# Kernel optimization log

Measured on AMD Instinct MI355X. Metric: run time of the kernel, lower is better.

The kernel has to match this reference:

```python
import jax, jax.numpy as jnp
import numpy as np

# decoded layout constants
NN, NO, SD = 16, 8, 4          # num_neighbors, num_obstacles, state_dim_per_agent
B = 131072                      # batch rows
H1, E, HP, AD = 64, 16, 64, 2   # phi hidden, embed, psi hidden, action dim
D_ROBOT, D_OBST = 0.3, 0.3
B_GAMMA, B_EXPH = 0.05, 1.0
PHI_MIN, PHI_MAX = -2.0, 2.0
A_MAX = 2.0


def setup_inputs() -> dict:
    key = jax.random.key(0)
    kx, kw = jax.random.split(key)
    # x: [count | goal(SD) | NN neighbor rel-states (SD each) | NO obstacle rel-pos (2 each)]
    x = jax.random.normal(kx, (B, 1 + SD + SD * NN + 2 * NO), dtype=jnp.float32) * 2.0
    x = x.at[:, 0].set(float(NN))
    names = [("Wp1n", (SD, H1)), ("bp1n", (H1,)), ("Wp2n", (H1, E)), ("bp2n", (E,)),
             ("Wr1n", (E, H1)), ("br1n", (H1,)), ("Wr2n", (H1, E)), ("br2n", (E,)),
             ("Wp1o", (2, H1)), ("bp1o", (H1,)), ("Wp2o", (H1, E)), ("bp2o", (E,)),
             ("Wr1o", (E, H1)), ("br1o", (H1,)), ("Wr2o", (H1, E)), ("br2o", (E,)),
             ("Wpsi1", (2 * E + SD, HP)), ("bpsi1", (HP,)), ("Wpsi2", (HP, AD)), ("bpsi2", (AD,))]
    ks = jax.random.split(kw, len(names))
    inp = {"x": x}
    for (n, sh), k in zip(names, ks):
        s = 1.0 / np.sqrt(sh[0])  # torch Linear default init scale
        inp[n] = jax.random.uniform(k, sh, jnp.float32, -s, s)
    return inp


def _mlp2(h, W1, b1, W2, b2):
    # Feedforward: activation between layers, linear output
    return jax.nn.relu(h @ W1 + b1) @ W2 + b2


def _deepset(el, Wp1, bp1, Wp2, bp2, Wr1, br1, Wr2, br2):
    # el: [B, n, d] -> phi each element, sum over set, rho
    phi = _mlp2(el, Wp1, bp1, Wp2, bp2)          # [B, n, E]
    return _mlp2(phi.sum(axis=1), Wr1, br1, Wr2, br2)  # [B, E]


def _barrier_sum(P, D):
    # P: [B, n, 2]; APF barrier gamma * P / (|P| * (|P|-D)^exph), summed over n
    nrm = jnp.linalg.norm(P, axis=-1, keepdims=True)   # [B, n, 1]
    H = nrm - D
    return (B_GAMMA * P / (nrm * H ** B_EXPH)).sum(axis=1)  # [B, 2]


def reference(x, Wp1n, bp1n, Wp2n, bp2n, Wr1n, br1n, Wr2n, br2n,
              Wp1o, bp1o, Wp2o, bp2o, Wr1o, br1o, Wr2o, br2o,
              Wpsi1, bpsi1, Wpsi2, bpsi2):
    nb = x.shape[0]
    g = x[:, 1:1 + SD]                                        # goal
    nbr = x[:, 1 + SD:1 + SD + SD * NN].reshape(nb, NN, SD)   # neighbor rel-states
    obs = x[:, 1 + SD + SD * NN:].reshape(nb, NO, 2)          # obstacle rel-pos

    rho_n = _deepset(nbr, Wp1n, bp1n, Wp2n, bp2n, Wr1n, br1n, Wr2n, br2n)
    rho_o = _deepset(obs, Wp1o, bp1o, Wp2o, bp2o, Wr1o, br1o, Wr2o, br2o)

    h = jnp.concatenate([rho_n, rho_o, g], axis=1)            # [B, 2E+SD]
    emp = _mlp2(h, Wpsi1, bpsi1, Wpsi2, bpsi2)                # psi network
    emp = (jnp.tanh(emp) + 1.0) / 2.0 * (PHI_MAX - PHI_MIN) + PHI_MIN  # scale_empty

    bar = _barrier_sum(-nbr[:, :, :2], D_ROBOT) + _barrier_sum(-obs, D_OBST)

    action = emp + bar
    # scale(): divide rows whose inf-norm exceeds a_max
    inv_alpha = jnp.maximum(jnp.max(jnp.abs(action), axis=1, keepdims=True) / A_MAX, 1.0)
    return action / inv_alpha
```

## Files before the change

### kernel.cpp

```cpp
#include <hip/hip_runtime.h>
#include <math.h>


typedef __attribute__((ext_vector_type(8))) _Float16 f16x8;
typedef __attribute__((ext_vector_type(2))) __fp16 fp16x2;
typedef __attribute__((ext_vector_type(4))) float f32x4;

#define XW 85
#define WPB 4

#define FR_S1N  0
#define FR_S1O  4
#define FR_G2N  8
#define FR_G2O  10
#define FR_RNA  12
#define FR_RNB  16
#define FR_ROA  18
#define FR_ROB  22
#define FR_PSI1 24
#define FR_PSI2 32
#define N_FRAGS 34

#define BIG_STR 144
#define PHI_STR 80
#define CAT_STR 144
#define L_BIG 0
#define L_PHI 2304
#define L_CAT 3584
#define L_OUT 5888
#define L_BAR 6016
#define WAVE_LDS 6144

__device__ __forceinline__ float fast_rcp(float x)  { return __builtin_amdgcn_rcpf(x); }
__device__ __forceinline__ float fast_sqrt(float x) { return __builtin_amdgcn_sqrtf(x); }

__device__ __forceinline__ float two_tanh(float a) {
    float ax = fabsf(a);
    float e = __expf(2.0f * ax);
    float t = 1.0f - 2.0f * fast_rcp(e + 1.0f);
    return copysignf(2.0f * t, a);
}

__device__ __forceinline__ void lds_order() {
    __asm__ __volatile__("" ::: "memory");
}

__device__ __forceinline__ unsigned pk2(float a, float b) {
    union { fp16x2 h; unsigned u; } t;
    t.h = __builtin_amdgcn_cvt_pkrtz(a, b);
    return t.u;
}
__device__ __forceinline__ f16x8 make_a4(float f0, float f1, float f2, float f3) {
    union { unsigned u[4]; f16x8 v; } U;
    U.u[0] = pk2(f0, f1); U.u[1] = pk2(f2, f3); U.u[2] = 0; U.u[3] = 0;
    return U.v;
}
__device__ __forceinline__ f16x8 make_a2(float f0, float f1) {
    union { unsigned u[4]; f16x8 v; } U;
    U.u[0] = pk2(f0, f1); U.u[1] = 0; U.u[2] = 0; U.u[3] = 0;
    return U.v;
}
__device__ __forceinline__ f16x8 lds_af(const char* area, int stride, int off, int lane) {
    int mm = lane & 15, qq = lane >> 4;
    return *(const f16x8*)(area + mm * stride + off + qq * 16);
}
__device__ __forceinline__ f16x8 load_bh(const _Float16* wsf, int frag, int lane) {
    return ((const f16x8*)(wsf + (size_t)frag * 512))[lane];
}
__device__ __forceinline__ f32x4 cinit(float b) {
    f32x4 c; c[0] = b; c[1] = b; c[2] = b; c[3] = b; return c;
}
__device__ __forceinline__ f32x4 mfma1(f16x8 a, f16x8 b, f32x4 c) {
    return __builtin_amdgcn_mfma_f32_16x16x32_f16(a, b, c, 0, 0, 0);
}

__global__ void bn_prep(const float* __restrict__ Wp1n, const float* __restrict__ Wp2n,
                        const float* __restrict__ Wr1n, const float* __restrict__ Wr2n,
                        const float* __restrict__ Wp1o, const float* __restrict__ Wp2o,
                        const float* __restrict__ Wr1o, const float* __restrict__ Wr2o,
                        const float* __restrict__ Wpsi1, const float* __restrict__ Wpsi2,
                        _Float16* __restrict__ wsf)
{
    int f = blockIdx.x;
    int lane = threadIdx.x;
    const float* W; int K, N, kk = 0, nt = 0, rel;
    if (f < 4)        { W = Wp1n;  K = 4;  N = 64; nt = f; }
    else if (f < 8)   { W = Wp1o;  K = 2;  N = 64; nt = f - 4; }
    else if (f < 10)  { W = Wp2n;  K = 64; N = 16; kk = f - 8; }
    else if (f < 12)  { W = Wp2o;  K = 64; N = 16; kk = f - 10; }
    else if (f < 16)  { W = Wr1n;  K = 16; N = 64; nt = f - 12; }
    else if (f < 18)  { W = Wr2n;  K = 64; N = 16; kk = f - 16; }
    else if (f < 22)  { W = Wr1o;  K = 16; N = 64; nt = f - 18; }
    else if (f < 24)  { W = Wr2o;  K = 64; N = 16; kk = f - 22; }
    else if (f < 32)  { rel = f - 24; W = Wpsi1; K = 36; N = 64; kk = rel >> 2; nt = rel & 3; }
    else              { W = Wpsi2; K = 64; N = 2;  kk = f - 32; }

    int q = lane >> 4, c = lane & 15;
    _Float16* dst = wsf + (size_t)f * 512 + lane * 8;
    for (int j = 0; j < 8; ++j) {
        int k = kk * 32 + q * 8 + j;
        int n = nt * 16 + c;
        float v = (k < K && n < N) ? W[k * N + n] : 0.f;
        dst[j] = (_Float16)v;
    }
}

__global__ __launch_bounds__(256) void bn_main(
    const float* __restrict__ x, const _Float16* __restrict__ wsf,
    const float* __restrict__ bp1n, const float* __restrict__ bp2n,
    const float* __restrict__ br1n, const float* __restrict__ br2n,
    const float* __restrict__ bp1o, const float* __restrict__ bp2o,
    const float* __restrict__ br1o, const float* __restrict__ br2o,
    const float* __restrict__ bpsi1, const float* __restrict__ bpsi2,
    float* __restrict__ out, int nb)
{
    __shared__ char smem[WPB * WAVE_LDS];
    const int lane = threadIdx.x & 63;
    const int wid  = threadIdx.x >> 6;
    const int group = blockIdx.x * WPB + wid;
    const int row0 = group * 16;
    if (row0 >= nb) return;

    char* Wl   = smem + wid * WAVE_LDS;
    char* BIG  = Wl + L_BIG;
    char* PHI  = Wl + L_PHI;
    char* CAT  = Wl + L_CAT;
    char* OUTA = Wl + L_OUT;
    char* BAR  = Wl + L_BAR;

    const int m = lane & 15, q = lane >> 4, c = m;
    const float* xrow = x + (size_t)(row0 + m) * XW;

    for (int i = lane; i < 128; i += 64) {
        int r = i >> 3, d = i & 7;
        *(unsigned*)(PHI + r * PHI_STR + 32 + d * 4) = 0;
    }
    for (int i = lane; i < 256; i += 64) {
        int r = i >> 4, d = i & 15;
        *(unsigned*)(CAT + r * CAT_STR + 64 + d * 4) = 0;
    }
    lds_order();

    {
        float bx = 0.f, by = 0.f;
        #pragma unroll
        for (int i = 0; i < 4; ++i) {
            int n = 4 * q + i;
            float px = -xrow[5 + 4 * n], py = -xrow[6 + 4 * n];
            float nrm = fast_sqrt(px * px + py * py);
            float coef = 0.05f * fast_rcp(nrm * (nrm - 0.3f));
            bx = fmaf(coef, px, bx);
            by = fmaf(coef, py, by);
        }
        #pragma unroll
        for (int i = 0; i < 2; ++i) {
            int o = 2 * q + i;
            float px = -xrow[69 + 2 * o], py = -xrow[70 + 2 * o];
            float nrm = fast_sqrt(px * px + py * py);
            float coef = 0.05f * fast_rcp(nrm * (nrm - 0.3f));
            bx = fmaf(coef, px, bx);
            by = fmaf(coef, py, by);
        }
        bx += __shfl_xor(bx, 16); by += __shfl_xor(by, 16);
        bx += __shfl_xor(bx, 32); by += __shfl_xor(by, 32);
        if (q == 0) { float2 bb; bb.x = bx; bb.y = by; *(float2*)(BAR + m * 8) = bb; }
    }

    if (lane < 16) {
        const float* xr = x + (size_t)(row0 + lane) * XW;
        uint2 gv;
        gv.x = pk2(xr[1], xr[2]);
        gv.y = pk2(xr[3], xr[4]);
        *(uint2*)(CAT + lane * CAT_STR + 64) = gv;
    }

    float b_s1n[4], b_s1o[4], b_rna[4], b_roa[4], b_p1[4];
    #pragma unroll
    for (int nt = 0; nt < 4; ++nt) {
        b_s1n[nt] = bp1n[nt * 16 + c];
        b_s1o[nt] = bp1o[nt * 16 + c];
        b_rna[nt] = br1n[nt * 16 + c];
        b_roa[nt] = br1o[nt * 16 + c];
        b_p1[nt]  = bpsi1[nt * 16 + c];
    }
    float b_g2n = 16.f * bp2n[c];
    float b_g2o = 8.f * bp2o[c];
    float b_rnb = br2n[c];
    float b_rob = br2o[c];
    float b_p2  = (c < 2) ? bpsi2[c] : 0.f;

    f16x8 Bs1n[4], Bg2n[2];
    #pragma unroll
    for (int nt = 0; nt < 4; ++nt) Bs1n[nt] = load_bh(wsf, FR_S1N + nt, lane);
    Bg2n[0] = load_bh(wsf, FR_G2N + 0, lane);
    Bg2n[1] = load_bh(wsf, FR_G2N + 1, lane);

    {
        f32x4 acc[4];
        #pragma unroll
        for (int nt = 0; nt < 4; ++nt) acc[nt] = cinit(0.f);
        float p0 = xrow[5], p1 = xrow[6], p2 = xrow[7], p3 = xrow[8];
        #pragma unroll 4
        for (int mm = 0; mm < 16; ++mm) {
            float n0, n1, n2, n3;
            if (mm + 1 < 16) {
                const float* xn = xrow + 5 + 4 * (mm + 1);
                n0 = xn[0]; n1 = xn[1]; n2 = xn[2]; n3 = xn[3];
            }
            f16x8 A = make_a4(p0, p1, p2, p3);
            #pragma unroll
            for (int nt = 0; nt < 4; ++nt) {
                f32x4 cc = mfma1(A, Bs1n[nt], cinit(b_s1n[nt]));
                #pragma unroll
                for (int reg = 0; reg < 4; ++reg)
                    acc[nt][reg] += fmaxf(cc[reg], 0.f);
            }
            if (mm + 1 < 16) { p0 = n0; p1 = n1; p2 = n2; p3 = n3; }
        }
        #pragma unroll
        for (int nt = 0; nt < 4; ++nt)
            #pragma unroll
            for (int reg = 0; reg < 4; ++reg)
                *(_Float16*)(BIG + (q * 4 + reg) * BIG_STR + (nt * 16 + c) * 2)
                    = (_Float16)acc[nt][reg];
    }
    f16x8 Brna[4];
    #pragma unroll
    for (int nt = 0; nt < 4; ++nt) Brna[nt] = load_bh(wsf, FR_RNA + nt, lane);
    lds_order();

    {
        f16x8 A0 = lds_af(BIG, BIG_STR, 0, lane);
        f16x8 A1 = lds_af(BIG, BIG_STR, 64, lane);
        f32x4 ca = mfma1(A0, Bg2n[0], cinit(b_g2n));
        f32x4 cb = mfma1(A1, Bg2n[1], cinit(0.f));
        #pragma unroll
        for (int reg = 0; reg < 4; ++reg)
            *(_Float16*)(PHI + (q * 4 + reg) * PHI_STR + c * 2) = (_Float16)(ca[reg] + cb[reg]);
    }
    f16x8 Brnb[2], Bs1o[4];
    Brnb[0] = load_bh(wsf, FR_RNB + 0, lane);
    Brnb[1] = load_bh(wsf, FR_RNB + 1, lane);
    #pragma unroll
    for (int nt = 0; nt < 4; ++nt) Bs1o[nt] = load_bh(wsf, FR_S1O + nt, lane);
    lds_order();

    {
        f16x8 A = lds_af(PHI, PHI_STR, 0, lane);
        #pragma unroll
        for (int nt = 0; nt < 4; ++nt) {
            f32x4 cc = mfma1(A, Brna[nt], cinit(b_rna[nt]));
            #pragma unroll
            for (int reg = 0; reg < 4; ++reg)
                *(_Float16*)(BIG + (q * 4 + reg) * BIG_STR + (nt * 16 + c) * 2) = (_Float16)fmaxf(cc[reg], 0.f);
        }
    }
    f16x8 Bg2o[2];
    Bg2o[0] = load_bh(wsf, FR_G2O + 0, lane);
    Bg2o[1] = load_bh(wsf, FR_G2O + 1, lane);
    lds_order();

    {
        f16x8 A0 = lds_af(BIG, BIG_STR, 0, lane);
        f16x8 A1 = lds_af(BIG, BIG_STR, 64, lane);
        f32x4 ca = mfma1(A0, Brnb[0], cinit(b_rnb));
        f32x4 cb = mfma1(A1, Brnb[1], cinit(0.f));
        #pragma unroll
        for (int reg = 0; reg < 4; ++reg)
            *(_Float16*)(CAT + (q * 4 + reg) * CAT_STR + c * 2) = (_Float16)(ca[reg] + cb[reg]);
    }
    f16x8 Broa[4];
    #pragma unroll
    for (int nt = 0; nt < 4; ++nt) Broa[nt] = load_bh(wsf, FR_ROA + nt, lane);
    lds_order();

    {
        f32x4 acc[4];
        #pragma unroll
        for (int nt = 0; nt < 4; ++nt) acc[nt] = cinit(0.f);
        #pragma unroll
        for (int oo = 0; oo < 8; ++oo) {
            f16x8 A = make_a2(xrow[69 + 2 * oo], xrow[70 + 2 * oo]);
            #pragma unroll
            for (int nt = 0; nt < 4; ++nt) {
                f32x4 cc = mfma1(A, Bs1o[nt], cinit(b_s1o[nt]));
                #pragma unroll
                for (int reg = 0; reg < 4; ++reg)
                    acc[nt][reg] += fmaxf(cc[reg], 0.f);
            }
        }
        #pragma unroll
        for (int nt = 0; nt < 4; ++nt)
            #pragma unroll
            for (int reg = 0; reg < 4; ++reg)
                *(_Float16*)(BIG + (q * 4 + reg) * BIG_STR + (nt * 16 + c) * 2)
                    = (_Float16)acc[nt][reg];
    }
    f16x8 Brob[2];
    Brob[0] = load_bh(wsf, FR_ROB + 0, lane);
    Brob[1] = load_bh(wsf, FR_ROB + 1, lane);
    lds_order();

    {
        f16x8 A0 = lds_af(BIG, BIG_STR, 0, lane);
        f16x8 A1 = lds_af(BIG, BIG_STR, 64, lane);
        f32x4 ca = mfma1(A0, Bg2o[0], cinit(b_g2o));
        f32x4 cb = mfma1(A1, Bg2o[1], cinit(0.f));
        #pragma unroll
        for (int reg = 0; reg < 4; ++reg)
            *(_Float16*)(PHI + (q * 4 + reg) * PHI_STR + c * 2) = (_Float16)(ca[reg] + cb[reg]);
    }
    f16x8 Bp1a[4];
    #pragma unroll
    for (int nt = 0; nt < 4; ++nt) Bp1a[nt] = load_bh(wsf, FR_PSI1 + nt, lane);
    lds_order();

    {
        f16x8 A = lds_af(PHI, PHI_STR, 0, lane);
        #pragma unroll
        for (int nt = 0; nt < 4; ++nt) {
            f32x4 cc = mfma1(A, Broa[nt], cinit(b_roa[nt]));
            #pragma unroll
            for (int reg = 0; reg < 4; ++reg)
                *(_Float16*)(BIG + (q * 4 + reg) * BIG_STR + (nt * 16 + c) * 2) = (_Float16)fmaxf(cc[reg], 0.f);
        }
    }
    f16x8 Bp1b[4], Bp2[2];
    #pragma unroll
    for (int nt = 0; nt < 4; ++nt) Bp1b[nt] = load_bh(wsf, FR_PSI1 + 4 + nt, lane);
    Bp2[0] = load_bh(wsf, FR_PSI2 + 0, lane);
    Bp2[1] = load_bh(wsf, FR_PSI2 + 1, lane);
    lds_order();

    {
        f16x8 A0 = lds_af(BIG, BIG_STR, 0, lane);
        f16x8 A1 = lds_af(BIG, BIG_STR, 64, lane);
        f32x4 ca = mfma1(A0, Brob[0], cinit(b_rob));
        f32x4 cb = mfma1(A1, Brob[1], cinit(0.f));
        #pragma unroll
        for (int reg = 0; reg < 4; ++reg)
            *(_Float16*)(CAT + (q * 4 + reg) * CAT_STR + (16 + c) * 2) = (_Float16)(ca[reg] + cb[reg]);
    }
    lds_order();

    {
        f16x8 A0 = lds_af(CAT, CAT_STR, 0, lane);
        f16x8 A1 = lds_af(CAT, CAT_STR, 64, lane);
        #pragma unroll
        for (int nt = 0; nt < 4; ++nt) {
            f32x4 ca = mfma1(A0, Bp1a[nt], cinit(b_p1[nt]));
            f32x4 cb = mfma1(A1, Bp1b[nt], cinit(0.f));
            #pragma unroll
            for (int reg = 0; reg < 4; ++reg)
                *(_Float16*)(BIG + (q * 4 + reg) * BIG_STR + (nt * 16 + c) * 2) = (_Float16)fmaxf(ca[reg] + cb[reg], 0.f);
        }
    }
    lds_order();

    {
        f16x8 A0 = lds_af(BIG, BIG_STR, 0, lane);
        f16x8 A1 = lds_af(BIG, BIG_STR, 64, lane);
        f32x4 ca = mfma1(A0, Bp2[0], cinit(b_p2));
        f32x4 cb = mfma1(A1, Bp2[1], cinit(0.f));
        if (c < 2) {
            #pragma unroll
            for (int reg = 0; reg < 4; ++reg)
                *(float*)(OUTA + (q * 4 + reg) * 8 + c * 4) = ca[reg] + cb[reg];
        }
    }
    lds_order();

    if (lane < 16) {
        float2 a  = *(const float2*)(OUTA + lane * 8);
        float2 bb = *(const float2*)(BAR + lane * 8);
        float a0 = two_tanh(a.x) + bb.x;
        float a1 = two_tanh(a.y) + bb.y;
        float amax = fmaxf(fabsf(a0), fabsf(a1));
        float inv_alpha = fmaxf(amax * 0.5f, 1.0f);
        float rr = fast_rcp(inv_alpha);
        float2 o; o.x = a0 * rr; o.y = a1 * rr;
        *(float2*)(out + (size_t)(row0 + lane) * 2) = o;
    }
}

extern "C" void kernel_launch(void* const* d_in, const int* in_sizes, int n_in,
                              void* d_out, int out_size, void* d_ws, size_t ws_size,
                              hipStream_t stream) {
    const float* x     = (const float*)d_in[0];
    const float* Wp1n  = (const float*)d_in[1];
    const float* bp1n  = (const float*)d_in[2];
    const float* Wp2n  = (const float*)d_in[3];
    const float* bp2n  = (const float*)d_in[4];
    const float* Wr1n  = (const float*)d_in[5];
    const float* br1n  = (const float*)d_in[6];
    const float* Wr2n  = (const float*)d_in[7];
    const float* br2n  = (const float*)d_in[8];
    const float* Wp1o  = (const float*)d_in[9];
    const float* bp1o  = (const float*)d_in[10];
    const float* Wp2o  = (const float*)d_in[11];
    const float* bp2o  = (const float*)d_in[12];
    const float* Wr1o  = (const float*)d_in[13];
    const float* br1o  = (const float*)d_in[14];
    const float* Wr2o  = (const float*)d_in[15];
    const float* br2o  = (const float*)d_in[16];
    const float* Wpsi1 = (const float*)d_in[17];
    const float* bpsi1 = (const float*)d_in[18];
    const float* Wpsi2 = (const float*)d_in[19];
    const float* bpsi2 = (const float*)d_in[20];
    float* out = (float*)d_out;

    int nb = in_sizes[0] / XW;
    _Float16* wsf = (_Float16*)d_ws;

    bn_prep<<<N_FRAGS, 64, 0, stream>>>(Wp1n, Wp2n, Wr1n, Wr2n,
                                        Wp1o, Wp2o, Wr1o, Wr2o,
                                        Wpsi1, Wpsi2, wsf);

    int groups = (nb + 15) / 16;
    int blocks = (groups + WPB - 1) / WPB;
    bn_main<<<blocks, 256, 0, stream>>>(x, wsf,
                                        bp1n, bp2n, br1n, br2n,
                                        bp1o, bp2o, br1o, br2o,
                                        bpsi1, bpsi2, out, nb);
}
```

Before: 156.3 us.

## Stage input rows in LDS with coalesced loads and interleave neighbor/obstacle deepsets

Each wave now loads its 16 input rows (340 uint4) into LDS with coalesced 16-byte loads. Strided per-lane global reads, which touched each row's 85 floats separately, now read from LDS instead. The neighbor and obstacle deepset pipelines are interleaved with separate LDS buffers, so independent MFMA chains overlap and there are fewer serialized phases. The cost is LDS per wave rising from about 6 KB to 15 KB, which may reduce occupancy, and more registers live at once.

Result: slower. 184.5 us (+18.0%).

```diff
diff --git a/kernel.cpp b/kernel.cpp
--- a/kernel.cpp
+++ b/kernel.cpp
@@ -21,15 +21,19 @@
 #define FR_PSI2 32
 #define N_FRAGS 34
 
+#define X_STR   340
 #define BIG_STR 144
 #define PHI_STR 80
 #define CAT_STR 144
-#define L_BIG 0
-#define L_PHI 2304
-#define L_CAT 3584
-#define L_OUT 5888
-#define L_BAR 6016
-#define WAVE_LDS 6144
+#define L_XBUF 0
+#define L_BIGN 5504
+#define L_BIGO 7808
+#define L_PHN  10112
+#define L_PHO  11392
+#define L_CAT  12672
+#define L_OUT  14976
+#define L_BAR  15104
+#define WAVE_LDS 15360
 
 __device__ __forceinline__ float fast_rcp(float x)  { return __builtin_amdgcn_rcpf(x); }
 __device__ __forceinline__ float fast_sqrt(float x) { return __builtin_amdgcn_sqrtf(x); }
@@ -122,57 +126,42 @@
     if (row0 >= nb) return;
 
     char* Wl   = smem + wid * WAVE_LDS;
-    char* BIG  = Wl + L_BIG;
-    char* PHI  = Wl + L_PHI;
+    char* XB   = Wl + L_XBUF;
+    char* BIGN = Wl + L_BIGN;
+    char* BIGO = Wl + L_BIGO;
+    char* PHN  = Wl + L_PHN;
+    char* PHO  = Wl + L_PHO;
     char* CAT  = Wl + L_CAT;
     char* OUTA = Wl + L_OUT;
     char* BAR  = Wl + L_BAR;
 
     const int m = lane & 15, q = lane >> 4, c = m;
-    const float* xrow = x + (size_t)(row0 + m) * XW;
+
+    {
+        const uint4* xb = (const uint4*)(x + (size_t)row0 * XW);
+        uint4 t[6];
+        #pragma unroll
+        for (int cch = 0; cch < 6; ++cch) {
+            int idx = cch * 64 + lane;
+            if (idx < 340) t[cch] = xb[idx];
+        }
+        #pragma unroll
+        for (int cch = 0; cch < 6; ++cch) {
+            int idx = cch * 64 + lane;
+            if (idx < 340) *(uint4*)(XB + idx * 16) = t[cch];
+        }
+    }
 
     for (int i = lane; i < 128; i += 64) {
         int r = i >> 3, d = i & 7;
-        *(unsigned*)(PHI + r * PHI_STR + 32 + d * 4) = 0;
+        *(unsigned*)(PHN + r * PHI_STR + 32 + d * 4) = 0;
+        *(unsigned*)(PHO + r * PHI_STR + 32 + d * 4) = 0;
     }
     for (int i = lane; i < 256; i += 64) {
         int r = i >> 4, d = i & 15;
         *(unsigned*)(CAT + r * CAT_STR + 64 + d * 4) = 0;
     }
     lds_order();
-
-    {
-        float bx = 0.f, by = 0.f;
-        #pragma unroll
-        for (int i = 0; i < 4; ++i) {
-            int n = 4 * q + i;
-            float px = -xrow[5 + 4 * n], py = -xrow[6 + 4 * n];
-            float nrm = fast_sqrt(px * px + py * py);
-            float coef = 0.05f * fast_rcp(nrm * (nrm - 0.3f));
-            bx = fmaf(coef, px, bx);
-            by = fmaf(coef, py, by);
-        }
-        #pragma unroll
-        for (int i = 0; i < 2; ++i) {
-            int o = 2 * q + i;
-            float px = -xrow[69 + 2 * o], py = -xrow[70 + 2 * o];
-            float nrm = fast_sqrt(px * px + py * py);
-            float coef = 0.05f * fast_rcp(nrm * (nrm - 0.3f));
-            bx = fmaf(coef, px, bx);
-            by = fmaf(coef, py, by);
-        }
-        bx += __shfl_xor(bx, 16); by += __shfl_xor(by, 16);
-        bx += __shfl_xor(bx, 32); by += __shfl_xor(by, 32);
-        if (q == 0) { float2 bb; bb.x = bx; bb.y = by; *(float2*)(BAR + m * 8) = bb; }
-    }
-
-    if (lane < 16) {
-        const float* xr = x + (size_t)(row0 + lane) * XW;
-        uint2 gv;
-        gv.x = pk2(xr[1], xr[2]);
-        gv.y = pk2(xr[3], xr[4]);
-        *(uint2*)(CAT + lane * CAT_STR + 64) = gv;
-    }
 
     float b_s1n[4], b_s1o[4], b_rna[4], b_roa[4], b_p1[4];
     #pragma unroll
@@ -189,158 +178,155 @@
     float b_rob = br2o[c];
     float b_p2  = (c < 2) ? bpsi2[c] : 0.f;
 
-    f16x8 Bs1n[4], Bg2n[2];
+    f16x8 Bs1n[4], Bs1o[4], Bg2n[2], Bg2o[2];
     #pragma unroll
     for (int nt = 0; nt < 4; ++nt) Bs1n[nt] = load_bh(wsf, FR_S1N + nt, lane);
+    #pragma unroll
+    for (int nt = 0; nt < 4; ++nt) Bs1o[nt] = load_bh(wsf, FR_S1O + nt, lane);
     Bg2n[0] = load_bh(wsf, FR_G2N + 0, lane);
     Bg2n[1] = load_bh(wsf, FR_G2N + 1, lane);
-
-    {
-        f32x4 acc[4];
-        #pragma unroll
-        for (int nt = 0; nt < 4; ++nt) acc[nt] = cinit(0.f);
-        float p0 = xrow[5], p1 = xrow[6], p2 = xrow[7], p3 = xrow[8];
-        #pragma unroll 4
+    Bg2o[0] = load_bh(wsf, FR_G2O + 0, lane);
+    Bg2o[1] = load_bh(wsf, FR_G2O + 1, lane);
+
+    const float* XR = (const float*)(XB + m * X_STR);
+
+    {
+        float bx = 0.f, by = 0.f;
+        #pragma unroll
+        for (int i = 0; i < 4; ++i) {
+            int n = 4 * q + i;
+            float px = -XR[5 + 4 * n], py = -XR[6 + 4 * n];
+            float nrm = fast_sqrt(px * px + py * py);
+            float coef = 0.05f * fast_rcp(nrm * (nrm - 0.3f));
+            bx = fmaf(coef, px, bx);
+            by = fmaf(coef, py, by);
+        }
+        #pragma unroll
+        for (int i = 0; i < 2; ++i) {
+            int o = 2 * q + i;
+            float px = -XR[69 + 2 * o], py = -XR[70 + 2 * o];
+            float nrm = fast_sqrt(px * px + py * py);
+            float coef = 0.05f * fast_rcp(nrm * (nrm - 0.3f));
+            bx = fmaf(coef, px, bx);
+            by = fmaf(coef, py, by);
+        }
+        bx += __shfl_xor(bx, 16); by += __shfl_xor(by, 16);
+        bx += __shfl_xor(bx, 32); by += __shfl_xor(by, 32);
+        if (q == 0) { float2 bb; bb.x = bx; bb.y = by; *(float2*)(BAR + m * 8) = bb; }
+    }
+
+    if (lane < 16) {
+        const float* xr = (const float*)(XB + lane * X_STR);
+        uint2 gv;
+        gv.x = pk2(xr[1], xr[2]);
+        gv.y = pk2(xr[3], xr[4]);
+        *(uint2*)(CAT + lane * CAT_STR + 64) = gv;
+    }
+
+    {
+        f32x4 accN[4], accO[4];
+        #pragma unroll
+        for (int nt = 0; nt < 4; ++nt) { accN[nt] = cinit(0.f); accO[nt] = cinit(0.f); }
+
+        #pragma unroll
+        for (int oo = 0; oo < 8; ++oo) {
+            f16x8 A = make_a2(XR[69 + 2 * oo], XR[70 + 2 * oo]);
+            #pragma unroll
+            for (int nt = 0; nt < 4; ++nt) {
+                f32x4 cc = mfma1(A, Bs1o[nt], cinit(b_s1o[nt]));
+                #pragma unroll
+                for (int reg = 0; reg < 4; ++reg)
+                    accO[nt][reg] += fmaxf(cc[reg], 0.f);
+            }
+        }
+        #pragma unroll 8
         for (int mm = 0; mm < 16; ++mm) {
-            float n0, n1, n2, n3;
-            if (mm + 1 < 16) {
-                const float* xn = xrow + 5 + 4 * (mm + 1);
-                n0 = xn[0]; n1 = xn[1]; n2 = xn[2]; n3 = xn[3];
-            }
-            f16x8 A = make_a4(p0, p1, p2, p3);
+            const float* e = XR + 5 + 4 * mm;
+            f16x8 A = make_a4(e[0], e[1], e[2], e[3]);
             #pragma unroll
             for (int nt = 0; nt < 4; ++nt) {
                 f32x4 cc = mfma1(A, Bs1n[nt], cinit(b_s1n[nt]));
                 #pragma unroll
                 for (int reg = 0; reg < 4; ++reg)
-                    acc[nt][reg] += fmaxf(cc[reg], 0.f);
+                    accN[nt][reg] += fmaxf(cc[reg], 0.f);
             }
-            if (mm + 1 < 16) { p0 = n0; p1 = n1; p2 = n2; p3 = n3; }
         }
         #pragma unroll
         for (int nt = 0; nt < 4; ++nt)
             #pragma unroll
-            for (int reg = 0; reg < 4; ++reg)
-                *(_Float16*)(BIG + (q * 4 + reg) * BIG_STR + (nt * 16 + c) * 2)
-                    = (_Float16)acc[nt][reg];
-    }
-    f16x8 Brna[4];
+            for (int reg = 0; reg < 4; ++reg) {
+                *(_Float16*)(BIGN + (q * 4 + reg) * BIG_STR + (nt * 16 + c) * 2) = (_Float16)accN[nt][reg];
+                *(_Float16*)(BIGO + (q * 4 + reg) * BIG_STR + (nt * 16 + c) * 2) = (_Float16)accO[nt][reg];
+            }
+    }
+    f16x8 Brna[4], Broa[4];
     #pragma unroll
     for (int nt = 0; nt < 4; ++nt) Brna[nt] = load_bh(wsf, FR_RNA + nt, lane);
-    lds_order();
-
-    {
-        f16x8 A0 = lds_af(BIG, BIG_STR, 0, lane);
-        f16x8 A1 = lds_af(BIG, BIG_STR, 64, lane);
-        f32x4 ca = mfma1(A0, Bg2n[0], cinit(b_g2n));
-        f32x4 cb = mfma1(A1, Bg2n[1], cinit(0.f));
-        #pragma unroll
-        for (int reg = 0; reg < 4; ++reg)
-            *(_Float16*)(PHI + (q * 4 + reg) * PHI_STR + c * 2) = (_Float16)(ca[reg] + cb[reg]);
-    }
-    f16x8 Brnb[2], Bs1o[4];
+    #pragma unroll
+    for (int nt = 0; nt < 4; ++nt) Broa[nt] = load_bh(wsf, FR_ROA + nt, lane);
+    lds_order();
+
+    {
+        f16x8 An0 = lds_af(BIGN, BIG_STR, 0, lane);
+        f16x8 An1 = lds_af(BIGN, BIG_STR, 64, lane);
+        f16x8 Ao0 = lds_af(BIGO, BIG_STR, 0, lane);
+        f16x8 Ao1 = lds_af(BIGO, BIG_STR, 64, lane);
+        f32x4 cn = mfma1(An0, Bg2n[0], cinit(b_g2n));
+        f32x4 co = mfma1(Ao0, Bg2o[0], cinit(b_g2o));
+        f32x4 cn1 = mfma1(An1, Bg2n[1], cinit(0.f));
+        f32x4 co1 = mfma1(Ao1, Bg2o[1], cinit(0.f));
+        #pragma unroll
+        for (int reg = 0; reg < 4; ++reg) {
+            *(_Float16*)(PHN + (q * 4 + reg) * PHI_STR + c * 2) = (_Float16)(cn[reg] + cn1[reg]);
+            *(_Float16*)(PHO + (q * 4 + reg) * PHI_STR + c * 2) = (_Float16)(co[reg] + co1[reg]);
+        }
+    }
+    f16x8 Brnb[2], Brob[2];
     Brnb[0] = load_bh(wsf, FR_RNB + 0, lane);
     Brnb[1] = load_bh(wsf, FR_RNB + 1, lane);
-    #pragma unroll
-    for (int nt = 0; nt < 4; ++nt) Bs1o[nt] = load_bh(wsf, FR_S1O + nt, lane);
-    lds_order();
-
-    {
-        f16x8 A = lds_af(PHI, PHI_STR, 0, lane);
-        #pragma unroll
-        for (int nt = 0; nt < 4; ++nt) {
-            f32x4 cc = mfma1(A, Brna[nt], cinit(b_rna[nt]));
-            #pragma unroll
-            for (int reg = 0; reg < 4; ++reg)
-                *(_Float16*)(BIG + (q * 4 + reg) * BIG_STR + (nt * 16 + c) * 2) = (_Float16)fmaxf(cc[reg], 0.f);
-        }
-    }
-    f16x8 Bg2o[2];
-    Bg2o[0] = load_bh(wsf, FR_G2O + 0, lane);
-    Bg2o[1] = load_bh(wsf, FR_G2O + 1, lane);
-    lds_order();
-
-    {
-        f16x8 A0 = lds_af(BIG, BIG_STR, 0, lane);
-        f16x8 A1 = lds_af(BIG, BIG_STR, 64, lane);
-        f32x4 ca = mfma1(A0, Brnb[0], cinit(b_rnb));
-        f32x4 cb = mfma1(A1, Brnb[1], cinit(0.f));
-        #pragma unroll
-        for (int reg = 0; reg < 4; ++reg)
-            *(_Float16*)(CAT + (q * 4 + reg) * CAT_STR + c * 2) = (_Float16)(ca[reg] + cb[reg]);
-    }
-    f16x8 Broa[4];
-    #pragma unroll
-    for (int nt = 0; nt < 4; ++nt) Broa[nt] = load_bh(wsf, FR_ROA + nt, lane);
-    lds_order();
-
-    {
-        f32x4 acc[4];
-        #pragma unroll
-        for (int nt = 0; nt < 4; ++nt) acc[nt] = cinit(0.f);
-        #pragma unroll
-        for (int oo = 0; oo < 8; ++oo) {
-            f16x8 A = make_a2(xrow[69 + 2 * oo], xrow[70 + 2 * oo]);
-            #pragma unroll
-            for (int nt = 0; nt < 4; ++nt) {
-                f32x4 cc = mfma1(A, Bs1o[nt], cinit(b_s1o[nt]));
-                #pragma unroll
-                for (int reg = 0; reg < 4; ++reg)
-                    acc[nt][reg] += fmaxf(cc[reg], 0.f);
-            }
-        }
-        #pragma unroll
-        for (int nt = 0; nt < 4; ++nt)
-            #pragma unroll
-            for (int reg = 0; reg < 4; ++reg)
-                *(_Float16*)(BIG + (q * 4 + reg) * BIG_STR + (nt * 16 + c) * 2)
-                    = (_Float16)acc[nt][reg];
-    }
-    f16x8 Brob[2];
     Brob[0] = load_bh(wsf, FR_ROB + 0, lane);
     Brob[1] = load_bh(wsf, FR_ROB + 1, lane);
     lds_order();
 
     {
-        f16x8 A0 = lds_af(BIG, BIG_STR, 0, lane);
-        f16x8 A1 = lds_af(BIG, BIG_STR, 64, lane);
-        f32x4 ca = mfma1(A0, Bg2o[0], cinit(b_g2o));
-        f32x4 cb = mfma1(A1, Bg2o[1], cinit(0.f));
-        #pragma unroll
-        for (int reg = 0; reg < 4; ++reg)
-            *(_Float16*)(PHI + (q * 4 + reg) * PHI_STR + c * 2) = (_Float16)(ca[reg] + cb[reg]);
-    }
-    f16x8 Bp1a[4];
+        f16x8 An = lds_af(PHN, PHI_STR, 0, lane);
+        f16x8 Ao = lds_af(PHO, PHI_STR, 0, lane);
+        #pragma unroll
+        for (int nt = 0; nt < 4; ++nt) {
+            f32x4 cn = mfma1(An, Brna[nt], cinit(b_rna[nt]));
+            f32x4 co = mfma1(Ao, Broa[nt], cinit(b_roa[nt]));
+            #pragma unroll
+            for (int reg = 0; reg < 4; ++reg) {
+                *(_Float16*)(BIGN + (q * 4 + reg) * BIG_STR + (nt * 16 + c) * 2) = (_Float16)fmaxf(cn[reg], 0.f);
+                *(_Float16*)(BIGO + (q * 4 + reg) * BIG_STR + (nt * 16 + c) * 2) = (_Float16)fmaxf(co[reg], 0.f);
+            }
+        }
+    }
+    f16x8 Bp1a[4], Bp1b[4];
     #pragma unroll
     for (int nt = 0; nt < 4; ++nt) Bp1a[nt] = load_bh(wsf, FR_PSI1 + nt, lane);
-    lds_order();
-
-    {
-        f16x8 A = lds_af(PHI, PHI_STR, 0, lane);
-        #pragma unroll
-        for (int nt = 0; nt < 4; ++nt) {
-            f32x4 cc = mfma1(A, Broa[nt], cinit(b_roa[nt]));
-            #pragma unroll
-            for (int reg = 0; reg < 4; ++reg)
-                *(_Float16*)(BIG + (q * 4 + reg) * BIG_STR + (nt * 16 + c) * 2) = (_Float16)fmaxf(cc[reg], 0.f);
-        }
-    }
-    f16x8 Bp1b[4], Bp2[2];
     #pragma unroll
     for (int nt = 0; nt < 4; ++nt) Bp1b[nt] = load_bh(wsf, FR_PSI1 + 4 + nt, lane);
+    lds_order();
+
+    {
+        f16x8 An0 = lds_af(BIGN, BIG_STR, 0, lane);
+        f16x8 An1 = lds_af(BIGN, BIG_STR, 64, lane);
+        f16x8 Ao0 = lds_af(BIGO, BIG_STR, 0, lane);
+        f16x8 Ao1 = lds_af(BIGO, BIG_STR, 64, lane);
+        f32x4 cn = mfma1(An0, Brnb[0], cinit(b_rnb));
+        f32x4 co = mfma1(Ao0, Brob[0], cinit(b_rob));
+        f32x4 cn1 = mfma1(An1, Brnb[1], cinit(0.f));
+        f32x4 co1 = mfma1(Ao1, Brob[1], cinit(0.f));
+        #pragma unroll
+        for (int reg = 0; reg < 4; ++reg) {
+            *(_Float16*)(CAT + (q * 4 + reg) * CAT_STR + c * 2)        = (_Float16)(cn[reg] + cn1[reg]);
+            *(_Float16*)(CAT + (q * 4 + reg) * CAT_STR + (16 + c) * 2) = (_Float16)(co[reg] + co1[reg]);
+        }
+    }
+    f16x8 Bp2[2];
     Bp2[0] = load_bh(wsf, FR_PSI2 + 0, lane);
     Bp2[1] = load_bh(wsf, FR_PSI2 + 1, lane);
-    lds_order();
-
-    {
-        f16x8 A0 = lds_af(BIG, BIG_STR, 0, lane);
-        f16x8 A1 = lds_af(BIG, BIG_STR, 64, lane);
-        f32x4 ca = mfma1(A0, Brob[0], cinit(b_rob));
-        f32x4 cb = mfma1(A1, Brob[1], cinit(0.f));
-        #pragma unroll
-        for (int reg = 0; reg < 4; ++reg)
-            *(_Float16*)(CAT + (q * 4 + reg) * CAT_STR + (16 + c) * 2) = (_Float16)(ca[reg] + cb[reg]);
-    }
     lds_order();
 
     {
@@ -352,14 +338,14 @@
             f32x4 cb = mfma1(A1, Bp1b[nt], cinit(0.f));
             #pragma unroll
             for (int reg = 0; reg < 4; ++reg)
-                *(_Float16*)(BIG + (q * 4 + reg) * BIG_STR + (nt * 16 + c) * 2) = (_Float16)fmaxf(ca[reg] + cb[reg], 0.f);
-        }
-    }
-    lds_order();
-
-    {
-        f16x8 A0 = lds_af(BIG, BIG_STR, 0, lane);
-        f16x8 A1 = lds_af(BIG, BIG_STR, 64, lane);
+                *(_Float16*)(BIGN + (q * 4 + reg) * BIG_STR + (nt * 16 + c) * 2) = (_Float16)fmaxf(ca[reg] + cb[reg], 0.f);
+        }
+    }
+    lds_order();
+
+    {
+        f16x8 A0 = lds_af(BIGN, BIG_STR, 0, lane);
+        f16x8 A1 = lds_af(BIGN, BIG_STR, 64, lane);
         f32x4 ca = mfma1(A0, Bp2[0], cinit(b_p2));
         f32x4 cb = mfma1(A1, Bp2[1], cinit(0.f));
         if (c < 2) {
```

## Split neighbor and obstacle deepsets across wave pairs per row group

Applied to the files above, without the earlier changes.

Each 16-row group is now handled by two waves instead of one. One wave computes the neighbor deepset, and the other computes the obstacle deepset, barrier and goal packing. After a block-wide barrier the second wave runs the psi network and the final scaling. This shortens the serial chain per row group and gives more parallelism. In exchange it adds a __syncthreads, leaves the neighbor wave idle during psi, uses more LDS per group, and removes the early-exit bounds check.

Result: faster. 151.2 us (-3.3%).

```diff
diff --git a/kernel.cpp b/kernel.cpp
--- a/kernel.cpp
+++ b/kernel.cpp
@@ -7,7 +7,6 @@
 typedef __attribute__((ext_vector_type(4))) float f32x4;
 
 #define XW 85
-#define WPB 4
 
 #define FR_S1N  0
 #define FR_S1O  4
@@ -24,12 +23,14 @@
 #define BIG_STR 144
 #define PHI_STR 80
 #define CAT_STR 144
-#define L_BIG 0
-#define L_PHI 2304
-#define L_CAT 3584
-#define L_OUT 5888
-#define L_BAR 6016
-#define WAVE_LDS 6144
+#define L_BIGN 0
+#define L_BIGO 2304
+#define L_PHN  4608
+#define L_PHO  5888
+#define L_CAT  7168
+#define L_OUT  9472
+#define L_BAR  9600
+#define GRP_LDS 9728
 
 __device__ __forceinline__ float fast_rcp(float x)  { return __builtin_amdgcn_rcpf(x); }
 __device__ __forceinline__ float fast_sqrt(float x) { return __builtin_amdgcn_sqrtf(x); }
@@ -114,272 +115,288 @@
     const float* __restrict__ bpsi1, const float* __restrict__ bpsi2,
     float* __restrict__ out, int nb)
 {
-    __shared__ char smem[WPB * WAVE_LDS];
+    __shared__ char smem[2 * GRP_LDS];
     const int lane = threadIdx.x & 63;
     const int wid  = threadIdx.x >> 6;
-    const int group = blockIdx.x * WPB + wid;
+    const int grp  = wid >> 1;
+    const int role = wid & 1;
+    const int group = blockIdx.x * 2 + grp;
     const int row0 = group * 16;
-    if (row0 >= nb) return;
-
-    char* Wl   = smem + wid * WAVE_LDS;
-    char* BIG  = Wl + L_BIG;
-    char* PHI  = Wl + L_PHI;
-    char* CAT  = Wl + L_CAT;
-    char* OUTA = Wl + L_OUT;
-    char* BAR  = Wl + L_BAR;
+
+    char* Gl   = smem + grp * GRP_LDS;
+    char* BIGN = Gl + L_BIGN;
+    char* BIGO = Gl + L_BIGO;
+    char* PHN  = Gl + L_PHN;
+    char* PHO  = Gl + L_PHO;
+    char* CAT  = Gl + L_CAT;
+    char* OUTA = Gl + L_OUT;
+    char* BAR  = Gl + L_BAR;
 
     const int m = lane & 15, q = lane >> 4, c = m;
     const float* xrow = x + (size_t)(row0 + m) * XW;
 
-    for (int i = lane; i < 128; i += 64) {
-        int r = i >> 3, d = i & 7;
-        *(unsigned*)(PHI + r * PHI_STR + 32 + d * 4) = 0;
+    if (role == 0) {
+        for (int i = lane; i < 128; i += 64) {
+            int r = i >> 3, d = i & 7;
+            *(unsigned*)(PHN + r * PHI_STR + 32 + d * 4) = 0;
+        }
+        lds_order();
+
+        float b_s1n[4], b_rna[4];
+        #pragma unroll
+        for (int nt = 0; nt < 4; ++nt) {
+            b_s1n[nt] = bp1n[nt * 16 + c];
+            b_rna[nt] = br1n[nt * 16 + c];
+        }
+        float b_g2n = 16.f * bp2n[c];
+        float b_rnb = br2n[c];
+
+        f16x8 Bs1n[4], Bg2n[2];
+        #pragma unroll
+        for (int nt = 0; nt < 4; ++nt) Bs1n[nt] = load_bh(wsf, FR_S1N + nt, lane);
+        Bg2n[0] = load_bh(wsf, FR_G2N + 0, lane);
+        Bg2n[1] = load_bh(wsf, FR_G2N + 1, lane);
+
+        {
+            f32x4 acc[4];
+            #pragma unroll
+            for (int nt = 0; nt < 4; ++nt) acc[nt] = cinit(0.f);
+            #pragma unroll 8
+            for (int mm = 0; mm < 16; ++mm) {
+                const float* e = xrow + 5 + 4 * mm;
+                f16x8 A = make_a4(e[0], e[1], e[2], e[3]);
+                #pragma unroll
+                for (int nt = 0; nt < 4; ++nt) {
+                    f32x4 cc = mfma1(A, Bs1n[nt], cinit(b_s1n[nt]));
+                    #pragma unroll
+                    for (int reg = 0; reg < 4; ++reg)
+                        acc[nt][reg] += fmaxf(cc[reg], 0.f);
+                }
+            }
+            #pragma unroll
+            for (int nt = 0; nt < 4; ++nt)
+                #pragma unroll
+                for (int reg = 0; reg < 4; ++reg)
+                    *(_Float16*)(BIGN + (q * 4 + reg) * BIG_STR + (nt * 16 + c) * 2)
+                        = (_Float16)acc[nt][reg];
+        }
+        f16x8 Brna[4];
+        #pragma unroll
+        for (int nt = 0; nt < 4; ++nt) Brna[nt] = load_bh(wsf, FR_RNA + nt, lane);
+        lds_order();
+
+        {
+            f16x8 A0 = lds_af(BIGN, BIG_STR, 0, lane);
+            f16x8 A1 = lds_af(BIGN, BIG_STR, 64, lane);
+            f32x4 ca = mfma1(A0, Bg2n[0], cinit(b_g2n));
+            f32x4 cb = mfma1(A1, Bg2n[1], cinit(0.f));
+            #pragma unroll
+            for (int reg = 0; reg < 4; ++reg)
+                *(_Float16*)(PHN + (q * 4 + reg) * PHI_STR + c * 2) = (_Float16)(ca[reg] + cb[reg]);
+        }
+        f16x8 Brnb[2];
+        Brnb[0] = load_bh(wsf, FR_RNB + 0, lane);
+        Brnb[1] = load_bh(wsf, FR_RNB + 1, lane);
+        lds_order();
+
+        {
+            f16x8 A = lds_af(PHN, PHI_STR, 0, lane);
+            #pragma unroll
+            for (int nt = 0; nt < 4; ++nt) {
+                f32x4 cc = mfma1(A, Brna[nt], cinit(b_rna[nt]));
+                #pragma unroll
+                for (int reg = 0; reg < 4; ++reg)
+                    *(_Float16*)(BIGN + (q * 4 + reg) * BIG_STR + (nt * 16 + c) * 2) = (_Float16)fmaxf(cc[reg], 0.f);
+            }
+        }
+        lds_order();
+
+        {
+            f16x8 A0 = lds_af(BIGN, BIG_STR, 0, lane);
+            f16x8 A1 = lds_af(BIGN, BIG_STR, 64, lane);
+            f32x4 ca = mfma1(A0, Brnb[0], cinit(b_rnb));
+            f32x4 cb = mfma1(A1, Brnb[1], cinit(0.f));
+            #pragma unroll
+            for (int reg = 0; reg < 4; ++reg)
+                *(_Float16*)(CAT + (q * 4 + reg) * CAT_STR + c * 2) = (_Float16)(ca[reg] + cb[reg]);
+        }
+    } else {
+        for (int i = lane; i < 128; i += 64) {
+            int r = i >> 3, d = i & 7;
+            *(unsigned*)(PHO + r * PHI_STR + 32 + d * 4) = 0;
+        }
+        for (int i = lane; i < 256; i += 64) {
+            int r = i >> 4, d = i & 15;
+            *(unsigned*)(CAT + r * CAT_STR + 64 + d * 4) = 0;
+        }
+        lds_order();
+
+        if (lane < 16) {
+            const float* xr = x + (size_t)(row0 + lane) * XW;
+            uint2 gv;
+            gv.x = pk2(xr[1], xr[2]);
+            gv.y = pk2(xr[3], xr[4]);
+            *(uint2*)(CAT + lane * CAT_STR + 64) = gv;
+        }
+
+        {
+            float bx = 0.f, by = 0.f;
+            #pragma unroll
+            for (int i = 0; i < 4; ++i) {
+                int n = 4 * q + i;
+                float px = -xrow[5 + 4 * n], py = -xrow[6 + 4 * n];
+                float nrm = fast_sqrt(px * px + py * py);
+                float coef = 0.05f * fast_rcp(nrm * (nrm - 0.3f));
+                bx = fmaf(coef, px, bx);
+                by = fmaf(coef, py, by);
+            }
+            #pragma unroll
+            for (int i = 0; i < 2; ++i) {
+                int o = 2 * q + i;
+                float px = -xrow[69 + 2 * o], py = -xrow[70 + 2 * o];
+                float nrm = fast_sqrt(px * px + py * py);
+                float coef = 0.05f * fast_rcp(nrm * (nrm - 0.3f));
+                bx = fmaf(coef, px, bx);
+                by = fmaf(coef, py, by);
+            }
+            bx += __shfl_xor(bx, 16); by += __shfl_xor(by, 16);
+            bx += __shfl_xor(bx, 32); by += __shfl_xor(by, 32);
+            if (q == 0) { float2 bb; bb.x = bx; bb.y = by; *(float2*)(BAR + m * 8) = bb; }
+        }
+
+        float b_s1o[4], b_roa[4];
+        #pragma unroll
+        for (int nt = 0; nt < 4; ++nt) {
+            b_s1o[nt] = bp1o[nt * 16 + c];
+            b_roa[nt] = br1o[nt * 16 + c];
+        }
+        float b_g2o = 8.f * bp2o[c];
+        float b_rob = br2o[c];
+
+        f16x8 Bs1o[4], Bg2o[2];
+        #pragma unroll
+        for (int nt = 0; nt < 4; ++nt) Bs1o[nt] = load_bh(wsf, FR_S1O + nt, lane);
+        Bg2o[0] = load_bh(wsf, FR_G2O + 0, lane);
+        Bg2o[1] = load_bh(wsf, FR_G2O + 1, lane);
+
+        {
+            f32x4 acc[4];
+            #pragma unroll
+            for (int nt = 0; nt < 4; ++nt) acc[nt] = cinit(0.f);
+            #pragma unroll
+            for (int oo = 0; oo < 8; ++oo) {
+                f16x8 A = make_a2(xrow[69 + 2 * oo], xrow[70 + 2 * oo]);
+                #pragma unroll
+                for (int nt = 0; nt < 4; ++nt) {
+                    f32x4 cc = mfma1(A, Bs1o[nt], cinit(b_s1o[nt]));
+                    #pragma unroll
+                    for (int reg = 0; reg < 4; ++reg)
+                        acc[nt][reg] += fmaxf(cc[reg], 0.f);
+                }
+            }
+            #pragma unroll
+            for (int nt = 0; nt < 4; ++nt)
+                #pragma unroll
+                for (int reg = 0; reg < 4; ++reg)
+                    *(_Float16*)(BIGO + (q * 4 + reg) * BIG_STR + (nt * 16 + c) * 2)
+                        = (_Float16)acc[nt][reg];
+        }
+        f16x8 Broa[4];
+        #pragma unroll
+        for (int nt = 0; nt < 4; ++nt) Broa[nt] = load_bh(wsf, FR_ROA + nt, lane);
+        lds_order();
+
+        {
+            f16x8 A0 = lds_af(BIGO, BIG_STR, 0, lane);
+            f16x8 A1 = lds_af(BIGO, BIG_STR, 64, lane);
+            f32x4 ca = mfma1(A0, Bg2o[0], cinit(b_g2o));
+            f32x4 cb = mfma1(A1, Bg2o[1], cinit(0.f));
+            #pragma unroll
+            for (int reg = 0; reg < 4; ++reg)
+                *(_Float16*)(PHO + (q * 4 + reg) * PHI_STR + c * 2) = (_Float16)(ca[reg] + cb[reg]);
+        }
+        f16x8 Brob[2];
+        Brob[0] = load_bh(wsf, FR_ROB + 0, lane);
+        Brob[1] = load_bh(wsf, FR_ROB + 1, lane);
+        lds_order();
+
+        {
+            f16x8 A = lds_af(PHO, PHI_STR, 0, lane);
+            #pragma unroll
+            for (int nt = 0; nt < 4; ++nt) {
+                f32x4 cc = mfma1(A, Broa[nt], cinit(b_roa[nt]));
+                #pragma unroll
+                for (int reg = 0; reg < 4; ++reg)
+                    *(_Float16*)(BIGO + (q * 4 + reg) * BIG_STR + (nt * 16 + c) * 2) = (_Float16)fmaxf(cc[reg], 0.f);
+            }
+        }
+        lds_order();
+
+        {
+            f16x8 A0 = lds_af(BIGO, BIG_STR, 0, lane);
+            f16x8 A1 = lds_af(BIGO, BIG_STR, 64, lane);
+            f32x4 ca = mfma1(A0, Brob[0], cinit(b_rob));
+            f32x4 cb = mfma1(A1, Brob[1], cinit(0.f));
+            #pragma unroll
+            for (int reg = 0; reg < 4; ++reg)
+                *(_Float16*)(CAT + (q * 4 + reg) * CAT_STR + (16 + c) * 2) = (_Float16)(ca[reg] + cb[reg]);
+        }
     }
-    for (int i = lane; i < 256; i += 64) {
-        int r = i >> 4, d = i & 15;
-        *(unsigned*)(CAT + r * CAT_STR + 64 + d * 4) = 0;
-    }
-    lds_order();
-
-    {
-        float bx = 0.f, by = 0.f;
-        #pragma unroll
-        for (int i = 0; i < 4; ++i) {
-            int n = 4 * q + i;
-            float px = -xrow[5 + 4 * n], py = -xrow[6 + 4 * n];
-            float nrm = fast_sqrt(px * px + py * py);
-            float coef = 0.05f * fast_rcp(nrm * (nrm - 0.3f));
-            bx = fmaf(coef, px, bx);
-            by = fmaf(coef, py, by);
-        }
-        #pragma unroll
-        for (int i = 0; i < 2; ++i) {
-            int o = 2 * q + i;
-            float px = -xrow[69 + 2 * o], py = -xrow[70 + 2 * o];
-            float nrm = fast_sqrt(px * px + py * py);
-            float coef = 0.05f * fast_rcp(nrm * (nrm - 0.3f));
-            bx = fmaf(coef, px, bx);
-            by = fmaf(coef, py, by);
-        }
-        bx += __shfl_xor(bx, 16); by += __shfl_xor(by, 16);
-        bx += __shfl_xor(bx, 32); by += __shfl_xor(by, 32);
-        if (q == 0) { float2 bb; bb.x = bx; bb.y = by; *(float2*)(BAR + m * 8) = bb; }
-    }
-
-    if (lane < 16) {
-        const float* xr = x + (size_t)(row0 + lane) * XW;
-        uint2 gv;
-        gv.x = pk2(xr[1], xr[2]);
-        gv.y = pk2(xr[3], xr[4]);
-        *(uint2*)(CAT + lane * CAT_STR + 64) = gv;
-    }
-
-    float b_s1n[4], b_s1o[4], b_rna[4], b_roa[4], b_p1[4];
-    #pragma unroll
-    for (int nt = 0; nt < 4; ++nt) {
-        b_s1n[nt] = bp1n[nt * 16 + c];
-        b_s1o[nt] = bp1o[nt * 16 + c];
-        b_rna[nt] = br1n[nt * 16 + c];
-        b_roa[nt] = br1o[nt * 16 + c];
-        b_p1[nt]  = bpsi1[nt * 16 + c];
-    }
-    float b_g2n = 16.f * bp2n[c];
-    float b_g2o = 8.f * bp2o[c];
-    float b_rnb = br2n[c];
-    float b_rob = br2o[c];
-    float b_p2  = (c < 2) ? bpsi2[c] : 0.f;
-
-    f16x8 Bs1n[4], Bg2n[2];
-    #pragma unroll
-    for (int nt = 0; nt < 4; ++nt) Bs1n[nt] = load_bh(wsf, FR_S1N + nt, lane);
-    Bg2n[0] = load_bh(wsf, FR_G2N + 0, lane);
-    Bg2n[1] = load_bh(wsf, FR_G2N + 1, lane);
-
-    {
-        f32x4 acc[4];
-        #pragma unroll
-        for (int nt = 0; nt < 4; ++nt) acc[nt] = cinit(0.f);
-        float p0 = xrow[5], p1 = xrow[6], p2 = xrow[7], p3 = xrow[8];
-        #pragma unroll 4
-        for (int mm = 0; mm < 16; ++mm) {
-            float n0, n1, n2, n3;
-            if (mm + 1 < 16) {
-                const float* xn = xrow + 5 + 4 * (mm + 1);
-                n0 = xn[0]; n1 = xn[1]; n2 = xn[2]; n3 = xn[3];
-            }
-            f16x8 A = make_a4(p0, p1, p2, p3);
+
+    __syncthreads();
+
+    if (role == 1) {
+        float b_p1[4];
+        #pragma unroll
+        for (int nt = 0; nt < 4; ++nt) b_p1[nt] = bpsi1[nt * 16 + c];
+        float b_p2 = (c < 2) ? bpsi2[c] : 0.f;
+
+        f16x8 Bp1a[4], Bp1b[4], Bp2[2];
+        #pragma unroll
+        for (int nt = 0; nt < 4; ++nt) Bp1a[nt] = load_bh(wsf, FR_PSI1 + nt, lane);
+        #pragma unroll
+        for (int nt = 0; nt < 4; ++nt) Bp1b[nt] = load_bh(wsf, FR_PSI1 + 4 + nt, lane);
+        Bp2[0] = load_bh(wsf, FR_PSI2 + 0, lane);
+        Bp2[1] = load_bh(wsf, FR_PSI2 + 1, lane);
+
+        {
+            f16x8 A0 = lds_af(CAT, CAT_STR, 0, lane);
+            f16x8 A1 = lds_af(CAT, CAT_STR, 64, lane);
             #pragma unroll
             for (int nt = 0; nt < 4; ++nt) {
-                f32x4 cc = mfma1(A, Bs1n[nt], cinit(b_s1n[nt]));
-                #pragma unroll
-                for (int reg = 0; reg < 4; ++reg)
-                    acc[nt][reg] += fmaxf(cc[reg], 0.f);
-            }
-            if (mm + 1 < 16) { p0 = n0; p1 = n1; p2 = n2; p3 = n3; }
-        }
-        #pragma unroll
-        for (int nt = 0; nt < 4; ++nt)
-            #pragma unroll
-            for (int reg = 0; reg < 4; ++reg)
-                *(_Float16*)(BIG + (q * 4 + reg) * BIG_STR + (nt * 16 + c) * 2)
-                    = (_Float16)acc[nt][reg];
-    }
-    f16x8 Brna[4];
-    #pragma unroll
-    for (int nt = 0; nt < 4; ++nt) Brna[nt] = load_bh(wsf, FR_RNA + nt, lane);
-    lds_order();
-
-    {
-        f16x8 A0 = lds_af(BIG, BIG_STR, 0, lane);
-        f16x8 A1 = lds_af(BIG, BIG_STR, 64, lane);
-        f32x4 ca = mfma1(A0, Bg2n[0], cinit(b_g2n));
-        f32x4 cb = mfma1(A1, Bg2n[1], cinit(0.f));
-        #pragma unroll
-        for (int reg = 0; reg < 4; ++reg)
-            *(_Float16*)(PHI + (q * 4 + reg) * PHI_STR + c * 2) = (_Float16)(ca[reg] + cb[reg]);
-    }
-    f16x8 Brnb[2], Bs1o[4];
-    Brnb[0] = load_bh(wsf, FR_RNB + 0, lane);
-    Brnb[1] = load_bh(wsf, FR_RNB + 1, lane);
-    #pragma unroll
-    for (int nt = 0; nt < 4; ++nt) Bs1o[nt] = load_bh(wsf, FR_S1O + nt, lane);
-    lds_order();
-
-    {
-        f16x8 A = lds_af(PHI, PHI_STR, 0, lane);
-        #pragma unroll
-        for (int nt = 0; nt < 4; ++nt) {
-            f32x4 cc = mfma1(A, Brna[nt], cinit(b_rna[nt]));
-            #pragma unroll
-            for (int reg = 0; reg < 4; ++reg)
-                *(_Float16*)(BIG + (q * 4 + reg) * BIG_STR + (nt * 16 + c) * 2) = (_Float16)fmaxf(cc[reg], 0.f);
-        }
-    }
-    f16x8 Bg2o[2];
-    Bg2o[0] = load_bh(wsf, FR_G2O + 0, lane);
-    Bg2o[1] = load_bh(wsf, FR_G2O + 1, lane);
-    lds_order();
-
-    {
-        f16x8 A0 = lds_af(BIG, BIG_STR, 0, lane);
-        f16x8 A1 = lds_af(BIG, BIG_STR, 64, lane);
-        f32x4 ca = mfma1(A0, Brnb[0], cinit(b_rnb));
-        f32x4 cb = mfma1(A1, Brnb[1], cinit(0.f));
-        #pragma unroll
-        for (int reg = 0; reg < 4; ++reg)
-            *(_Float16*)(CAT + (q * 4 + reg) * CAT_STR + c * 2) = (_Float16)(ca[reg] + cb[reg]);
-    }
-    f16x8 Broa[4];
-    #pragma unroll
-    for (int nt = 0; nt < 4; ++nt) Broa[nt] = load_bh(wsf, FR_ROA + nt, lane);
-    lds_order();
-
-    {
-        f32x4 acc[4];
-        #pragma unroll
-        for (int nt = 0; nt < 4; ++nt) acc[nt] = cinit(0.f);
-        #pragma unroll
-        for (int oo = 0; oo < 8; ++oo) {
-            f16x8 A = make_a2(xrow[69 + 2 * oo], xrow[70 + 2 * oo]);
-            #pragma unroll
-            for (int nt = 0; nt < 4; ++nt) {
-                f32x4 cc = mfma1(A, Bs1o[nt], cinit(b_s1o[nt]));
-                #pragma unroll
-                for (int reg = 0; reg < 4; ++reg)
-                    acc[nt][reg] += fmaxf(cc[reg], 0.f);
-            }
-        }
-        #pragma unroll
-        for (int nt = 0; nt < 4; ++nt)
-            #pragma unroll
-            for (int reg = 0; reg < 4; ++reg)
-                *(_Float16*)(BIG + (q * 4 + reg) * BIG_STR + (nt * 16 + c) * 2)
-                    = (_Float16)acc[nt][reg];
-    }
-    f16x8 Brob[2];
-    Brob[0] = load_bh(wsf, FR_ROB + 0, lane);
-    Brob[1] = load_bh(wsf, FR_ROB + 1, lane);
-    lds_order();
-
-    {
-        f16x8 A0 = lds_af(BIG, BIG_STR, 0, lane);
-        f16x8 A1 = lds_af(BIG, BIG_STR, 64, lane);
-        f32x4 ca = mfma1(A0, Bg2o[0], cinit(b_g2o));
-        f32x4 cb = mfma1(A1, Bg2o[1], cinit(0.f));
-        #pragma unroll
-        for (int reg = 0; reg < 4; ++reg)
-            *(_Float16*)(PHI + (q * 4 + reg) * PHI_STR + c * 2) = (_Float16)(ca[reg] + cb[reg]);
-    }
-    f16x8 Bp1a[4];
-    #pragma unroll
-    for (int nt = 0; nt < 4; ++nt) Bp1a[nt] = load_bh(wsf, FR_PSI1 + nt, lane);
-    lds_order();
-
-    {
-        f16x8 A = lds_af(PHI, PHI_STR, 0, lane);
-        #pragma unroll
-        for (int nt = 0; nt < 4; ++nt) {
-            f32x4 cc = mfma1(A, Broa[nt], cinit(b_roa[nt]));
-            #pragma unroll
-            for (int reg = 0; reg < 4; ++reg)
-                *(_Float16*)(BIG + (q * 4 + reg) * BIG_STR + (nt * 16 + c) * 2) = (_Float16)fmaxf(cc[reg], 0.f);
-        }
-    }
-    f16x8 Bp1b[4], Bp2[2];
-    #pragma unroll
-    for (int nt = 0; nt < 4; ++nt) Bp1b[nt] = load_bh(wsf, FR_PSI1 + 4 + nt, lane);
-    Bp2[0] = load_bh(wsf, FR_PSI2 + 0, lane);
-    Bp2[1] = load_bh(wsf, FR_PSI2 + 1, lane);
-    lds_order();
-
-    {
-        f16x8 A0 = lds_af(BIG, BIG_STR, 0, lane);
-        f16x8 A1 = lds_af(BIG, BIG_STR, 64, lane);
-        f32x4 ca = mfma1(A0, Brob[0], cinit(b_rob));
-        f32x4 cb = mfma1(A1, Brob[1], cinit(0.f));
-        #pragma unroll
-        for (int reg = 0; reg < 4; ++reg)
-            *(_Float16*)(CAT + (q * 4 + reg) * CAT_STR + (16 + c) * 2) = (_Float16)(ca[reg] + cb[reg]);
-    }
-    lds_order();
-
-    {
-        f16x8 A0 = lds_af(CAT, CAT_STR, 0, lane);
-        f16x8 A1 = lds_af(CAT, CAT_STR, 64, lane);
-        #pragma unroll
-        for (int nt = 0; nt < 4; ++nt) {
-            f32x4 ca = mfma1(A0, Bp1a[nt], cinit(b_p1[nt]));
-            f32x4 cb = mfma1(A1, Bp1b[nt], cinit(0.f));
-            #pragma unroll
-            for (int reg = 0; reg < 4; ++reg)
-                *(_Float16*)(BIG + (q * 4 + reg) * BIG_STR + (nt * 16 + c) * 2) = (_Float16)fmaxf(ca[reg] + cb[reg], 0.f);
-        }
-    }
-    lds_order();
-
-    {
-        f16x8 A0 = lds_af(BIG, BIG_STR, 0, lane);
-        f16x8 A1 = lds_af(BIG, BIG_STR, 64, lane);
-        f32x4 ca = mfma1(A0, Bp2[0], cinit(b_p2));
-        f32x4 cb = mfma1(A1, Bp2[1], cinit(0.f));
-        if (c < 2) {
-            #pragma unroll
-            for (int reg = 0; reg < 4; ++reg)
-                *(float*)(OUTA + (q * 4 + reg) * 8 + c * 4) = ca[reg] + cb[reg];
-        }
-    }
-    lds_order();
-
-    if (lane < 16) {
-        float2 a  = *(const float2*)(OUTA + lane * 8);
-        float2 bb = *(const float2*)(BAR + lane * 8);
-        float a0 = two_tanh(a.x) + bb.x;
-        float a1 = two_tanh(a.y) + bb.y;
-        float amax = fmaxf(fabsf(a0), fabsf(a1));
-        float inv_alpha = fmaxf(amax * 0.5f, 1.0f);
-        float rr = fast_rcp(inv_alpha);
-        float2 o; o.x = a0 * rr; o.y = a1 * rr;
-        *(float2*)(out + (size_t)(row0 + lane) * 2) = o;
+                f32x4 ca = mfma1(A0, Bp1a[nt], cinit(b_p1[nt]));
+                f32x4 cb = mfma1(A1, Bp1b[nt], cinit(0.f));
+                #pragma unroll
+                for (int reg = 0; reg < 4; ++reg)
+                    *(_Float16*)(BIGO + (q * 4 + reg) * BIG_STR + (nt * 16 + c) * 2) = (_Float16)fmaxf(ca[reg] + cb[reg], 0.f);
+            }
+        }
+        lds_order();
+
+        {
+            f16x8 A0 = lds_af(BIGO, BIG_STR, 0, lane);
+            f16x8 A1 = lds_af(BIGO, BIG_STR, 64, lane);
+            f32x4 ca = mfma1(A0, Bp2[0], cinit(b_p2));
+            f32x4 cb = mfma1(A1, Bp2[1], cinit(0.f));
+            if (c < 2) {
+                #pragma unroll
+                for (int reg = 0; reg < 4; ++reg)
+                    *(float*)(OUTA + (q * 4 + reg) * 8 + c * 4) = ca[reg] + cb[reg];
+            }
+        }
+        lds_order();
+
+        if (lane < 16) {
+            float2 a  = *(const float2*)(OUTA + lane * 8);
+            float2 bb = *(const float2*)(BAR + lane * 8);
+            float a0 = two_tanh(a.x) + bb.x;
+            float a1 = two_tanh(a.y) + bb.y;
+            float amax = fmaxf(fabsf(a0), fabsf(a1));
+            float inv_alpha = fmaxf(amax * 0.5f, 1.0f);
+            float rr = fast_rcp(inv_alpha);
+            float2 o; o.x = a0 * rr; o.y = a1 * rr;
+            *(float2*)(out + (size_t)(row0 + lane) * 2) = o;
+        }
     }
 }
 
@@ -417,7 +434,7 @@
                                         Wpsi1, Wpsi2, wsf);
 
     int groups = (nb + 15) / 16;
-    int blocks = (groups + WPB - 1) / WPB;
+    int blocks = (groups + 1) / 2;
     bn_main<<<blocks, 256, 0, stream>>>(x, wsf,
                                         bp1n, bp2n, br1n, br2n,
                                         bp1o, bp2o, br1o, br2o,
```
